# Kernel optimization log

Measured on AMD Instinct MI355X. Metric: run time of the kernel, lower is better.

## Reference

```python
import jax, jax.numpy as jnp
import numpy as np
from jax.nn import relu, softplus, sigmoid

B, T, C, L = 256, 128, 16, 64
ENC, H, OBS_IN, NLAGS = 32, 64, 8, 24
SUBSTEPS = 2


def setup_inputs() -> dict:
    key = jax.random.key(0)
    ks = jax.random.split(key, 32)
    rn = lambda k, shp, s=0.1: jax.random.normal(k, shp, dtype=jnp.float32) * s
    return {
        "timestamps": jnp.linspace(0.0, 1.0, T, dtype=jnp.float32),
        "obs": rn(ks[0], (B, NLAGS, OBS_IN), 1.0),
        "coef_d": rn(ks[1], (B, T - 1, C)),
        "coef_c": rn(ks[2], (B, T - 1, C)),
        "coef_b": rn(ks[3], (B, T - 1, C)),
        "coef_a": rn(ks[4], (B, T - 1, C)),
        "gru_wih": rn(ks[5], (3 * H, OBS_IN)),
        "gru_whh": rn(ks[6], (3 * H, H)),
        "gru_bih": rn(ks[7], (3 * H,)),
        "gru_bhh": rn(ks[8], (3 * H,)),
        "gru_lin_w": rn(ks[9], (ENC, H)),
        "ie_w0": rn(ks[10], (128, ENC + C)),
        "ie_b0": rn(ks[11], (128,)),
        "ie_wh": rn(ks[12], (1, 128, 128)),
        "ie_bh": rn(ks[13], (1, 128)),
        "ie_wout": rn(ks[14], (L, 128)),
        "ie_bout": rn(ks[15], (L,)),
        "vf_w0": rn(ks[16], (128, L)),
        "vf_b0": rn(ks[17], (128,)),
        "vf_wh": rn(ks[18], (1, 128, 128)),
        "vf_bh": rn(ks[19], (1, 128)),
        "vf_wout": rn(ks[20], (L * C, 128)),
        "vf_bout": rn(ks[21], (L * C,)),
        "dec_w0": rn(ks[22], (L // 2, L)),
        "dec_b0": rn(ks[23], (L // 2,)),
        "dec_wh": rn(ks[24], (1, L // 2, L // 2)),
        "dec_bh": rn(ks[25], (1, L // 2)),
        "dec_wout": rn(ks[26], (8, L // 2)),
        "dec_bout": rn(ks[27], (8,)),
    }


def _mlp(x, w0, b0, wh, bh, wout, bout, act, fact):
    h = act(w0 @ x + b0)
    for i in range(wh.shape[0]):  # fixed small depth
        h = act(wh[i] @ h + bh[i])
    return fact(wout @ h + bout)


_ident = lambda v: v


def reference(timestamps, obs, coef_d, coef_c, coef_b, coef_a,
              gru_wih, gru_whh, gru_bih, gru_bhh, gru_lin_w,
              ie_w0, ie_b0, ie_wh, ie_bh, ie_wout, ie_bout,
              vf_w0, vf_b0, vf_wh, vf_bh, vf_wout, vf_bout,
              dec_w0, dec_b0, dec_wh, dec_bh, dec_wout, dec_bout):

    def single(obs_s, d_s, c_s, b_s, a_s):
        # --- GRU observation encoder ---
        def cell(h, x):
            gi = gru_wih @ x + gru_bih
            gh = gru_whh @ h + gru_bhh
            ir, iz, inn = jnp.split(gi, 3)
            hr, hz, hn = jnp.split(gh, 3)
            r = sigmoid(ir + hr)
            z = sigmoid(iz + hz)
            n = jnp.tanh(inn + r * hn)
            return (1.0 - z) * n + z * h, None
        hT, _ = jax.lax.scan(cell, jnp.zeros((H,), jnp.float32), obs_s)
        enc = gru_lin_w @ hT
        # control.evaluate(t0): cubic poly at frac=0 -> constant coeff a[0]
        x0 = a_s[0]
        y0 = _mlp(jnp.concatenate([enc, x0]), ie_w0, ie_b0, ie_wh, ie_bh, ie_wout, ie_bout, relu, _ident)

        def vf(y):
            return _mlp(y, vf_w0, vf_b0, vf_wh, vf_bh, vf_wout, vf_bout, softplus, jnp.tanh).reshape(L, C)

        js = jnp.arange(SUBSTEPS, dtype=jnp.float32)

        def interval(y, xs):
            t0, t1, di, ci, bi = xs
            hstep = (t1 - t0) / SUBSTEPS
            def f(frac, yy):
                dx = bi + 2.0 * ci * frac + 3.0 * di * frac * frac  # dX/dt on this interval
                return vf(yy) @ dx  # (L,)
            def sub(yy, j):  # one fixed Dopri5 step
                f0 = j * hstep
                k1 = f(f0, yy)
                k2 = f(f0 + hstep / 5, yy + hstep * (k1 / 5))
                k3 = f(f0 + 3 * hstep / 10, yy + hstep * (3 / 40 * k1 + 9 / 40 * k2))
                k4 = f(f0 + 4 * hstep / 5, yy + hstep * (44 / 45 * k1 - 56 / 15 * k2 + 32 / 9 * k3))
                k5 = f(f0 + 8 * hstep / 9, yy + hstep * (19372 / 6561 * k1 - 25360 / 2187 * k2 + 64448 / 6561 * k3 - 212 / 729 * k4))
                k6 = f(f0 + hstep, yy + hstep * (9017 / 3168 * k1 - 355 / 33 * k2 + 46732 / 5247 * k3 + 49 / 176 * k4 - 5103 / 18656 * k5))
                yn = yy + hstep * (35 / 384 * k1 + 500 / 1113 * k3 + 125 / 192 * k4 - 2187 / 6784 * k5 + 11 / 84 * k6)
                return yn, None
            y, _ = jax.lax.scan(jax.checkpoint(sub), y, js)
            return y, y

        xs = (timestamps[:-1], timestamps[1:], d_s, c_s, b_s)
        _, ys_rest = jax.lax.scan(interval, y0, xs)
        ys = jnp.concatenate([y0[None], ys_rest], axis=0)  # (T, L)
        dec = lambda yy: _mlp(yy, dec_w0, dec_b0, dec_wh, dec_bh, dec_wout, dec_bout, relu, _ident)
        return jax.vmap(dec)(ys)  # (T, state_size)

    return jax.vmap(single)(obs, coef_d, coef_c, coef_b, coef_a)  # (B, T, state_size)
```

## Files before the change

kernel.cpp:

```cpp
#include <hip/hip_runtime.h>
#include <hip/hip_fp16.h>

#define TPB 512

typedef _Float16 h2v __attribute__((ext_vector_type(2)));

__device__ __forceinline__ float dot2f(unsigned int a, unsigned int b, float c) {
#if __has_builtin(__builtin_amdgcn_fdot2)
    return __builtin_amdgcn_fdot2(__builtin_bit_cast(h2v, a), __builtin_bit_cast(h2v, b), c, false);
#else
    float2 af = __half22float2(__builtin_bit_cast(__half2, a));
    float2 bf = __half22float2(__builtin_bit_cast(__half2, b));
    return fmaf(af.y, bf.y, fmaf(af.x, bf.x, c));
#endif
}

__device__ __forceinline__ unsigned int pack2(float a, float b) {
    unsigned int lo = (unsigned int)__half_as_ushort(__float2half_rn(a));
    unsigned int hi = (unsigned int)__half_as_ushort(__float2half_rn(b));
    return lo | (hi << 16);
}

__device__ __forceinline__ float softplus_f(float x) {
    return fmaxf(x, 0.f) + __logf(1.f + __expf(-fabsf(x)));
}
__device__ __forceinline__ float tanh_f(float x) {
    float e = __expf(2.f * x);
    return 1.f - 2.f / (e + 1.f);
}
__device__ __forceinline__ float sigmoid_f(float x) {
    return 1.f / (1.f + __expf(-x));
}

__global__ __launch_bounds__(TPB, 2) void ncde_kernel(
    const float* __restrict__ timestamps, const float* __restrict__ obs,
    const float* __restrict__ coef_d, const float* __restrict__ coef_c,
    const float* __restrict__ coef_b, const float* __restrict__ coef_a,
    const float* __restrict__ gru_wih, const float* __restrict__ gru_whh,
    const float* __restrict__ gru_bih, const float* __restrict__ gru_bhh,
    const float* __restrict__ gru_lin_w,
    const float* __restrict__ ie_w0, const float* __restrict__ ie_b0,
    const float* __restrict__ ie_wh, const float* __restrict__ ie_bh,
    const float* __restrict__ ie_wout, const float* __restrict__ ie_bout,
    const float* __restrict__ vf_w0, const float* __restrict__ vf_b0,
    const float* __restrict__ vf_wh, const float* __restrict__ vf_bh,
    const float* __restrict__ vf_wout, const float* __restrict__ vf_bout,
    const float* __restrict__ dec_w0, const float* __restrict__ dec_b0,
    const float* __restrict__ dec_wh, const float* __restrict__ dec_bh,
    const float* __restrict__ dec_wout, const float* __restrict__ dec_bout,
    float* __restrict__ out)
{
    const int b = blockIdx.x;
    const int tid = threadIdx.x;

    __shared__ __align__(16) float s_ysall[128][64];
    __shared__ __align__(16) float s_whh[192 * 65];
    __shared__ __align__(16) float s_wih[192 * 9];
    __shared__ __align__(16) float s_obs[24 * 8];
    __shared__ float s_gi[192];
    __shared__ float s_gh[192];
    __shared__ __align__(16) float s_y[64];
    __shared__ __align__(16) float s_ysg[64];
    __shared__ __align__(16) __half s_h1h[128];
    __shared__ __align__(16) __half s_h2h[128];
    __shared__ float s_k[6][64];
    __shared__ float s_bi[16], s_ci[16], s_di[16], s_dx[16];
    __shared__ __align__(16) float s_v48[48];
    __shared__ float s_m1[128], s_m2[128];
    __shared__ float s_A[6][5];
    __shared__ float s_C[6];
    __shared__ float s_Bw[6];

    if (tid == 0) {
        const float A[6][5] = {
            {0.f, 0.f, 0.f, 0.f, 0.f},
            {0.2f, 0.f, 0.f, 0.f, 0.f},
            {3.f / 40.f, 9.f / 40.f, 0.f, 0.f, 0.f},
            {44.f / 45.f, -56.f / 15.f, 32.f / 9.f, 0.f, 0.f},
            {19372.f / 6561.f, -25360.f / 2187.f, 64448.f / 6561.f, -212.f / 729.f, 0.f},
            {9017.f / 3168.f, -355.f / 33.f, 46732.f / 5247.f, 49.f / 176.f, -5103.f / 18656.f}};
        const float C[6] = {0.f, 0.2f, 0.3f, 0.8f, 8.f / 9.f, 1.f};
        const float Bw[6] = {35.f / 384.f, 0.f, 500.f / 1113.f, 125.f / 192.f,
                             -2187.f / 6784.f, 11.f / 84.f};
        for (int i = 0; i < 6; ++i) {
            s_C[i] = C[i];
            s_Bw[i] = Bw[i];
            for (int m = 0; m < 5; ++m) s_A[i][m] = A[i][m];
        }
    }

    for (int idx = tid; idx < 192 * 64; idx += TPB)
        s_whh[(idx >> 6) * 65 + (idx & 63)] = gru_whh[idx];
    for (int idx = tid; idx < 192 * 8; idx += TPB)
        s_wih[(idx >> 3) * 9 + (idx & 7)] = gru_wih[idx];
    for (int idx = tid; idx < 24 * 8; idx += TPB)
        s_obs[idx] = obs[(size_t)b * 192 + idx];
    const float bih_r = (tid < 192) ? gru_bih[tid] : 0.f;
    const float bhh_r = (tid < 192) ? gru_bhh[tid] : 0.f;
    if (tid < 64) s_y[tid] = 0.f;
    __syncthreads();

    for (int step = 0; step < 24; ++step) {
        if (tid < 192) {
            float gi = bih_r;
            const float* wr = &s_wih[tid * 9];
            const float* xr = &s_obs[step * 8];
#pragma unroll
            for (int j = 0; j < 8; ++j) gi = fmaf(wr[j], xr[j], gi);
            float gh = bhh_r;
            const float* hr = &s_whh[tid * 65];
            for (int j = 0; j < 64; ++j) gh = fmaf(hr[j], s_y[j], gh);
            s_gi[tid] = gi;
            s_gh[tid] = gh;
        }
        __syncthreads();
        if (tid < 64) {
            float rg = sigmoid_f(s_gi[tid] + s_gh[tid]);
            float zg = sigmoid_f(s_gi[64 + tid] + s_gh[64 + tid]);
            float ng = tanh_f(s_gi[128 + tid] + rg * s_gh[128 + tid]);
            s_y[tid] = (1.f - zg) * ng + zg * s_y[tid];
        }
        __syncthreads();
    }

    if (tid < 32) {
        float e = 0.f;
        const float* wr = gru_lin_w + tid * 64;
        for (int j = 0; j < 64; ++j) e = fmaf(wr[j], s_y[j], e);
        s_v48[tid] = e;
    } else if (tid < 48) {
        s_v48[tid] = coef_a[(size_t)b * 127 * 16 + (tid - 32)];
    }
    __syncthreads();

    if (tid < 128) {
        float a = ie_b0[tid];
        const float* wr = ie_w0 + tid * 48;
        for (int j = 0; j < 48; ++j) a = fmaf(wr[j], s_v48[j], a);
        s_m1[tid] = fmaxf(a, 0.f);
    }
    __syncthreads();
    if (tid < 128) {
        float a = ie_bh[tid];
        const float* wr = ie_wh + tid * 128;
        for (int j = 0; j < 128; ++j) a = fmaf(wr[j], s_m1[j], a);
        s_m2[tid] = fmaxf(a, 0.f);
    }
    __syncthreads();
    if (tid < 64) {
        float a = ie_bout[tid];
        const float* wr = ie_wout + tid * 128;
        for (int j = 0; j < 128; ++j) a = fmaf(wr[j], s_m2[j], a);
        s_y[tid] = a;
        s_ysall[0][tid] = a;
    }
    __syncthreads();

    const int qrow = tid >> 2, qc = tid & 3;
    float w0_r[16];
    {
        const float* base = vf_w0 + qrow * 64 + qc * 16;
#pragma unroll
        for (int j = 0; j < 16; ++j) w0_r[j] = base[j];
    }
    unsigned int wh_r[16];
    {
        const float* base = vf_wh + qrow * 128 + qc * 32;
#pragma unroll
        for (int j = 0; j < 16; ++j) wh_r[j] = pack2(base[2 * j], base[2 * j + 1]);
    }
    unsigned int wq0[64], wq1[64];
    {
        const float* r0 = vf_wout + (size_t)(2 * tid) * 128;
#pragma unroll
        for (int j = 0; j < 64; ++j) wq0[j] = pack2(r0[2 * j], r0[2 * j + 1]);
        const float* r1 = r0 + 128;
#pragma unroll
        for (int j = 0; j < 64; ++j) wq1[j] = pack2(r1[2 * j], r1[2 * j + 1]);
    }
    const float b0_r = vf_b0[qrow];
    const float bh_r = vf_bh[qrow];
    const float bo0 = vf_bout[2 * tid], bo1 = vf_bout[2 * tid + 1];
    const int l_idx = tid >> 3;
    const int c0 = 2 * (tid & 7);

    const size_t cofs = (size_t)b * 127 * 16;

#pragma unroll 1
    for (int t = 0; t < 127; ++t) {
        if (tid < 16) s_bi[tid] = coef_b[cofs + t * 16 + tid];
        else if (tid < 32) s_ci[tid - 16] = coef_c[cofs + t * 16 + (tid - 16)];
        else if (tid < 48) s_di[tid - 32] = coef_d[cofs + t * 16 + (tid - 32)];
        const float t0 = timestamps[t], t1 = timestamps[t + 1];
        const float hstep = (t1 - t0) * 0.5f;
        __syncthreads();

#pragma unroll 1
        for (int sub = 0; sub < 2; ++sub) {
            const float f0 = (float)sub * hstep;
#pragma unroll 1
            for (int s = 0; s < 6; ++s) {
                if (tid < 64) {
                    float yv = s_y[tid];
                    for (int m = 0; m < s; ++m)
                        yv = fmaf(hstep * s_A[s][m], s_k[m][tid], yv);
                    s_ysg[tid] = yv;
                } else if (tid < 80) {
                    int c = tid - 64;
                    float frac = fmaf(s_C[s], hstep, f0);
                    s_dx[c] = fmaf(3.f * s_di[c], frac * frac,
                                   fmaf(2.f * s_ci[c], frac, s_bi[c]));
                }
                __syncthreads();

                {
                    float a = 0.f;
                    const float* yb = &s_ysg[qc * 16];
#pragma unroll
                    for (int k4 = 0; k4 < 4; ++k4) {
                        float4 yv = *reinterpret_cast<const float4*>(yb + 4 * k4);
                        a = fmaf(w0_r[4 * k4 + 0], yv.x, a);
                        a = fmaf(w0_r[4 * k4 + 1], yv.y, a);
                        a = fmaf(w0_r[4 * k4 + 2], yv.z, a);
                        a = fmaf(w0_r[4 * k4 + 3], yv.w, a);
                    }
                    a += __shfl_xor(a, 1);
                    a += __shfl_xor(a, 2);
                    if (qc == 0) s_h1h[qrow] = __float2half_rn(softplus_f(a + b0_r));
                }
                __syncthreads();

                {
                    float a = 0.f;
                    const __half* hb = &s_h1h[qc * 32];
#pragma unroll
                    for (int k4 = 0; k4 < 4; ++k4) {
                        uint4 hv = *reinterpret_cast<const uint4*>(hb + 8 * k4);
                        a = dot2f(wh_r[4 * k4 + 0], hv.x, a);
                        a = dot2f(wh_r[4 * k4 + 1], hv.y, a);
                        a = dot2f(wh_r[4 * k4 + 2], hv.z, a);
                        a = dot2f(wh_r[4 * k4 + 3], hv.w, a);
                    }
                    a += __shfl_xor(a, 1);
                    a += __shfl_xor(a, 2);
                    if (qc == 0) s_h2h[qrow] = __float2half_rn(softplus_f(a + bh_r));
                }
                __syncthreads();

                {
                    float a0 = 0.f, a1 = 0.f;
#pragma unroll
                    for (int k4 = 0; k4 < 16; ++k4) {
                        uint4 hv = *reinterpret_cast<const uint4*>(&s_h2h[8 * k4]);
                        a0 = dot2f(wq0[4 * k4 + 0], hv.x, a0);
                        a1 = dot2f(wq1[4 * k4 + 0], hv.x, a1);
                        a0 = dot2f(wq0[4 * k4 + 1], hv.y, a0);
                        a1 = dot2f(wq1[4 * k4 + 1], hv.y, a1);
                        a0 = dot2f(wq0[4 * k4 + 2], hv.z, a0);
                        a1 = dot2f(wq1[4 * k4 + 2], hv.z, a1);
                        a0 = dot2f(wq0[4 * k4 + 3], hv.w, a0);
                        a1 = dot2f(wq1[4 * k4 + 3], hv.w, a1);
                    }
                    float v0 = tanh_f(a0 + bo0);
                    float v1 = tanh_f(a1 + bo1);
                    float p = v0 * s_dx[c0] + v1 * s_dx[c0 + 1];
                    p += __shfl_xor(p, 1);
                    p += __shfl_xor(p, 2);
                    p += __shfl_xor(p, 4);
                    if ((tid & 7) == 0) s_k[s][l_idx] = p;
                }
                __syncthreads();
            }

            if (tid < 64) {
                float yv = s_y[tid];
#pragma unroll
                for (int m = 0; m < 6; ++m)
                    yv = fmaf(hstep * s_Bw[m], s_k[m][tid], yv);
                s_y[tid] = yv;
                if (sub == 1) s_ysall[t + 1][tid] = yv;
            }
            __syncthreads();
        }
    }

    const int wid = tid >> 6, lane = tid & 63;
    for (int t = wid; t < 128; t += 8) {
        const float* yy = s_ysall[t];
        float h1d = 0.f;
        if (lane < 32) {
            float a = dec_b0[lane];
            const float* wr = dec_w0 + lane * 64;
            for (int j = 0; j < 64; ++j) a = fmaf(wr[j], yy[j], a);
            h1d = fmaxf(a, 0.f);
        }
        float a2 = (lane < 32) ? dec_bh[lane] : 0.f;
#pragma unroll 8
        for (int j = 0; j < 32; ++j) {
            float hj = __shfl(h1d, j);
            if (lane < 32) a2 = fmaf(dec_wh[lane * 32 + j], hj, a2);
        }
        float h2d = fmaxf(a2, 0.f);
        float o = (lane < 8) ? dec_bout[lane] : 0.f;
#pragma unroll 8
        for (int j = 0; j < 32; ++j) {
            float hj = __shfl(h2d, j);
            if (lane < 8) o = fmaf(dec_wout[lane * 32 + j], hj, o);
        }
        if (lane < 8) out[(size_t)b * 1024 + t * 8 + lane] = o;
    }
}

extern "C" void kernel_launch(void* const* d_in, const int* in_sizes, int n_in,
                              void* d_out, int out_size, void* d_ws, size_t ws_size,
                              hipStream_t stream) {
    const float* p[29];
    for (int i = 0; i < 29; ++i) p[i] = (const float*)d_in[i];
    ncde_kernel<<<256, TPB, 0, stream>>>(
        p[0], p[1], p[2], p[3], p[4], p[5], p[6], p[7], p[8], p[9], p[10],
        p[11], p[12], p[13], p[14], p[15], p[16], p[17], p[18], p[19], p[20],
        p[21], p[22], p[23], p[24], p[25], p[26], p[27], p[28],
        (float*)d_out);
}
```

Measured before the change: 2.705 ms.

## Double block to 1024 threads, one vf_wout row per thread, drop a barrier

The block grows from 512 to 1024 threads, and each thread now holds a single fp16 vf_wout row instead of two. This roughly halves per-thread register weight storage and serial dot-product length. The first two MLP layers use 8-way splits per row. The control derivative dx is computed inline per thread instead of through a separate shared-memory stage, and the stage-0 y copy is written at the end of the previous step, which removes one barrier per RK stage. The GRU loop uses four accumulators. The cost is more warps contending at every __syncthreads, plus higher per-block resource pressure under the new launch bounds.

```diff
diff --git a/kernel.cpp b/kernel.cpp
--- a/kernel.cpp
+++ b/kernel.cpp
@@ -1,7 +1,7 @@
 #include <hip/hip_runtime.h>
 #include <hip/hip_fp16.h>
 
-#define TPB 512
+#define TPB 1024
 
 typedef _Float16 h2v __attribute__((ext_vector_type(2)));
 
@@ -32,7 +32,7 @@
     return 1.f / (1.f + __expf(-x));
 }
 
-__global__ __launch_bounds__(TPB, 2) void ncde_kernel(
+__global__ __launch_bounds__(TPB, 4) void ncde_kernel(
     const float* __restrict__ timestamps, const float* __restrict__ obs,
     const float* __restrict__ coef_d, const float* __restrict__ coef_c,
     const float* __restrict__ coef_b, const float* __restrict__ coef_a,
@@ -64,7 +64,7 @@
     __shared__ __align__(16) __half s_h1h[128];
     __shared__ __align__(16) __half s_h2h[128];
     __shared__ float s_k[6][64];
-    __shared__ float s_bi[16], s_ci[16], s_di[16], s_dx[16];
+    __shared__ float s_bi[16], s_ci[16], s_di[16];
     __shared__ __align__(16) float s_v48[48];
     __shared__ float s_m1[128], s_m2[128];
     __shared__ float s_A[6][5];
@@ -93,8 +93,7 @@
         s_whh[(idx >> 6) * 65 + (idx & 63)] = gru_whh[idx];
     for (int idx = tid; idx < 192 * 8; idx += TPB)
         s_wih[(idx >> 3) * 9 + (idx & 7)] = gru_wih[idx];
-    for (int idx = tid; idx < 24 * 8; idx += TPB)
-        s_obs[idx] = obs[(size_t)b * 192 + idx];
+    if (tid < 24 * 8) s_obs[tid] = obs[(size_t)b * 192 + tid];
     const float bih_r = (tid < 192) ? gru_bih[tid] : 0.f;
     const float bhh_r = (tid < 192) ? gru_bhh[tid] : 0.f;
     if (tid < 64) s_y[tid] = 0.f;
@@ -107,11 +106,17 @@
             const float* xr = &s_obs[step * 8];
 #pragma unroll
             for (int j = 0; j < 8; ++j) gi = fmaf(wr[j], xr[j], gi);
-            float gh = bhh_r;
+            float g0 = bhh_r, g1 = 0.f, g2 = 0.f, g3 = 0.f;
             const float* hr = &s_whh[tid * 65];
-            for (int j = 0; j < 64; ++j) gh = fmaf(hr[j], s_y[j], gh);
+#pragma unroll 4
+            for (int j = 0; j < 64; j += 4) {
+                g0 = fmaf(hr[j + 0], s_y[j + 0], g0);
+                g1 = fmaf(hr[j + 1], s_y[j + 1], g1);
+                g2 = fmaf(hr[j + 2], s_y[j + 2], g2);
+                g3 = fmaf(hr[j + 3], s_y[j + 3], g3);
+            }
             s_gi[tid] = gi;
-            s_gh[tid] = gh;
+            s_gh[tid] = (g0 + g1) + (g2 + g3);
         }
         __syncthreads();
         if (tid < 64) {
@@ -152,37 +157,35 @@
         const float* wr = ie_wout + tid * 128;
         for (int j = 0; j < 128; ++j) a = fmaf(wr[j], s_m2[j], a);
         s_y[tid] = a;
+        s_ysg[tid] = a;
         s_ysall[0][tid] = a;
     }
     __syncthreads();
 
-    const int qrow = tid >> 2, qc = tid & 3;
-    float w0_r[16];
+    const int row8 = tid >> 3, seg8 = tid & 7;
+    float w0_r[8];
     {
-        const float* base = vf_w0 + qrow * 64 + qc * 16;
-#pragma unroll
-        for (int j = 0; j < 16; ++j) w0_r[j] = base[j];
-    }
-    unsigned int wh_r[16];
+        const float* base = vf_w0 + row8 * 64 + seg8 * 8;
+#pragma unroll
+        for (int j = 0; j < 8; ++j) w0_r[j] = base[j];
+    }
+    unsigned int wh_r[8];
     {
-        const float* base = vf_wh + qrow * 128 + qc * 32;
-#pragma unroll
-        for (int j = 0; j < 16; ++j) wh_r[j] = pack2(base[2 * j], base[2 * j + 1]);
-    }
-    unsigned int wq0[64], wq1[64];
+        const float* base = vf_wh + row8 * 128 + seg8 * 16;
+#pragma unroll
+        for (int j = 0; j < 8; ++j) wh_r[j] = pack2(base[2 * j], base[2 * j + 1]);
+    }
+    unsigned int wq[64];
     {
-        const float* r0 = vf_wout + (size_t)(2 * tid) * 128;
-#pragma unroll
-        for (int j = 0; j < 64; ++j) wq0[j] = pack2(r0[2 * j], r0[2 * j + 1]);
-        const float* r1 = r0 + 128;
-#pragma unroll
-        for (int j = 0; j < 64; ++j) wq1[j] = pack2(r1[2 * j], r1[2 * j + 1]);
-    }
-    const float b0_r = vf_b0[qrow];
-    const float bh_r = vf_bh[qrow];
-    const float bo0 = vf_bout[2 * tid], bo1 = vf_bout[2 * tid + 1];
-    const int l_idx = tid >> 3;
-    const int c0 = 2 * (tid & 7);
+        const float* r0 = vf_wout + (size_t)tid * 128;
+#pragma unroll
+        for (int j = 0; j < 64; ++j) wq[j] = pack2(r0[2 * j], r0[2 * j + 1]);
+    }
+    const float b0_r = vf_b0[row8];
+    const float bh_r = vf_bh[row8];
+    const float bo = vf_bout[tid];
+    const int l_idx = tid >> 4;
+    const int c_idx = tid & 15;
 
     const size_t cofs = (size_t)b * 127 * 16;
 
@@ -200,74 +203,75 @@
             const float f0 = (float)sub * hstep;
 #pragma unroll 1
             for (int s = 0; s < 6; ++s) {
-                if (tid < 64) {
-                    float yv = s_y[tid];
-                    for (int m = 0; m < s; ++m)
-                        yv = fmaf(hstep * s_A[s][m], s_k[m][tid], yv);
-                    s_ysg[tid] = yv;
-                } else if (tid < 80) {
-                    int c = tid - 64;
-                    float frac = fmaf(s_C[s], hstep, f0);
-                    s_dx[c] = fmaf(3.f * s_di[c], frac * frac,
-                                   fmaf(2.f * s_ci[c], frac, s_bi[c]));
+                if (s > 0) {
+                    if (tid < 64) {
+                        float yv = s_y[tid];
+                        for (int m = 0; m < s; ++m)
+                            yv = fmaf(hstep * s_A[s][m], s_k[m][tid], yv);
+                        s_ysg[tid] = yv;
+                    }
+                    __syncthreads();
+                }
+
+                {
+                    const float* yb = &s_ysg[seg8 * 8];
+                    float4 y0 = *reinterpret_cast<const float4*>(yb);
+                    float4 y1 = *reinterpret_cast<const float4*>(yb + 4);
+                    float a0 = w0_r[0] * y0.x, a1 = w0_r[1] * y0.y;
+                    a0 = fmaf(w0_r[2], y0.z, a0);
+                    a1 = fmaf(w0_r[3], y0.w, a1);
+                    a0 = fmaf(w0_r[4], y1.x, a0);
+                    a1 = fmaf(w0_r[5], y1.y, a1);
+                    a0 = fmaf(w0_r[6], y1.z, a0);
+                    a1 = fmaf(w0_r[7], y1.w, a1);
+                    float a = a0 + a1;
+                    a += __shfl_xor(a, 1);
+                    a += __shfl_xor(a, 2);
+                    a += __shfl_xor(a, 4);
+                    if (seg8 == 0) s_h1h[row8] = __float2half_rn(softplus_f(a + b0_r));
                 }
                 __syncthreads();
 
                 {
-                    float a = 0.f;
-                    const float* yb = &s_ysg[qc * 16];
-#pragma unroll
-                    for (int k4 = 0; k4 < 4; ++k4) {
-                        float4 yv = *reinterpret_cast<const float4*>(yb + 4 * k4);
-                        a = fmaf(w0_r[4 * k4 + 0], yv.x, a);
-                        a = fmaf(w0_r[4 * k4 + 1], yv.y, a);
-                        a = fmaf(w0_r[4 * k4 + 2], yv.z, a);
-                        a = fmaf(w0_r[4 * k4 + 3], yv.w, a);
-                    }
+                    const __half* hb = &s_h1h[seg8 * 16];
+                    uint4 h0 = *reinterpret_cast<const uint4*>(hb);
+                    uint4 h1v = *reinterpret_cast<const uint4*>(hb + 8);
+                    float a0 = dot2f(wh_r[0], h0.x, 0.f);
+                    float a1 = dot2f(wh_r[1], h0.y, 0.f);
+                    a0 = dot2f(wh_r[2], h0.z, a0);
+                    a1 = dot2f(wh_r[3], h0.w, a1);
+                    a0 = dot2f(wh_r[4], h1v.x, a0);
+                    a1 = dot2f(wh_r[5], h1v.y, a1);
+                    a0 = dot2f(wh_r[6], h1v.z, a0);
+                    a1 = dot2f(wh_r[7], h1v.w, a1);
+                    float a = a0 + a1;
                     a += __shfl_xor(a, 1);
                     a += __shfl_xor(a, 2);
-                    if (qc == 0) s_h1h[qrow] = __float2half_rn(softplus_f(a + b0_r));
+                    a += __shfl_xor(a, 4);
+                    if (seg8 == 0) s_h2h[row8] = __float2half_rn(softplus_f(a + bh_r));
                 }
                 __syncthreads();
 
                 {
-                    float a = 0.f;
-                    const __half* hb = &s_h1h[qc * 32];
-#pragma unroll
-                    for (int k4 = 0; k4 < 4; ++k4) {
-                        uint4 hv = *reinterpret_cast<const uint4*>(hb + 8 * k4);
-                        a = dot2f(wh_r[4 * k4 + 0], hv.x, a);
-                        a = dot2f(wh_r[4 * k4 + 1], hv.y, a);
-                        a = dot2f(wh_r[4 * k4 + 2], hv.z, a);
-                        a = dot2f(wh_r[4 * k4 + 3], hv.w, a);
-                    }
-                    a += __shfl_xor(a, 1);
-                    a += __shfl_xor(a, 2);
-                    if (qc == 0) s_h2h[qrow] = __float2half_rn(softplus_f(a + bh_r));
-                }
-                __syncthreads();
-
-                {
-                    float a0 = 0.f, a1 = 0.f;
+                    float a0 = 0.f, a1 = 0.f, a2 = 0.f, a3 = 0.f;
 #pragma unroll
                     for (int k4 = 0; k4 < 16; ++k4) {
                         uint4 hv = *reinterpret_cast<const uint4*>(&s_h2h[8 * k4]);
-                        a0 = dot2f(wq0[4 * k4 + 0], hv.x, a0);
-                        a1 = dot2f(wq1[4 * k4 + 0], hv.x, a1);
-                        a0 = dot2f(wq0[4 * k4 + 1], hv.y, a0);
-                        a1 = dot2f(wq1[4 * k4 + 1], hv.y, a1);
-                        a0 = dot2f(wq0[4 * k4 + 2], hv.z, a0);
-                        a1 = dot2f(wq1[4 * k4 + 2], hv.z, a1);
-                        a0 = dot2f(wq0[4 * k4 + 3], hv.w, a0);
-                        a1 = dot2f(wq1[4 * k4 + 3], hv.w, a1);
+                        a0 = dot2f(wq[4 * k4 + 0], hv.x, a0);
+                        a1 = dot2f(wq[4 * k4 + 1], hv.y, a1);
+                        a2 = dot2f(wq[4 * k4 + 2], hv.z, a2);
+                        a3 = dot2f(wq[4 * k4 + 3], hv.w, a3);
                     }
-                    float v0 = tanh_f(a0 + bo0);
-                    float v1 = tanh_f(a1 + bo1);
-                    float p = v0 * s_dx[c0] + v1 * s_dx[c0 + 1];
+                    float v = tanh_f((a0 + a1) + (a2 + a3) + bo);
+                    float frac = fmaf(s_C[s], hstep, f0);
+                    float dx = fmaf(3.f * s_di[c_idx], frac * frac,
+                                    fmaf(2.f * s_ci[c_idx], frac, s_bi[c_idx]));
+                    float p = v * dx;
                     p += __shfl_xor(p, 1);
                     p += __shfl_xor(p, 2);
                     p += __shfl_xor(p, 4);
-                    if ((tid & 7) == 0) s_k[s][l_idx] = p;
+                    p += __shfl_xor(p, 8);
+                    if (c_idx == 0) s_k[s][l_idx] = p;
                 }
                 __syncthreads();
             }
@@ -278,6 +282,7 @@
                 for (int m = 0; m < 6; ++m)
                     yv = fmaf(hstep * s_Bw[m], s_k[m][tid], yv);
                 s_y[tid] = yv;
+                s_ysg[tid] = yv;
                 if (sub == 1) s_ysall[t + 1][tid] = yv;
             }
             __syncthreads();
@@ -285,7 +290,7 @@
     }
 
     const int wid = tid >> 6, lane = tid & 63;
-    for (int t = wid; t < 128; t += 8) {
+    for (int t = wid; t < 128; t += 16) {
         const float* yy = s_ysall[t];
         float h1d = 0.f;
         if (lane < 32) {
```

Measured after the change: 3.438 ms. 27.1% more time.

## Batch 16 samples per block and run vector-field MLP on MFMA

Applied to the files above, without the earlier changes.

Each block now handles 16 batch samples instead of one, so grid size drops to 16 blocks. The three vector-field matvecs become 16x16x32 f16 MFMA matmuls, with weights kept in registers as fragments and activations stored in swizzled shared memory. The GRU encoder, initial MLP and per-step decoder are also batched, and decoding now runs inside the time loop. This amortises weights and barriers over 16 samples, but it leaves most CUs idle and puts a longer dependent chain in each block.

```diff
diff --git a/kernel.cpp b/kernel.cpp
--- a/kernel.cpp
+++ b/kernel.cpp
@@ -2,24 +2,10 @@
 #include <hip/hip_fp16.h>
 
 #define TPB 512
-
-typedef _Float16 h2v __attribute__((ext_vector_type(2)));
-
-__device__ __forceinline__ float dot2f(unsigned int a, unsigned int b, float c) {
-#if __has_builtin(__builtin_amdgcn_fdot2)
-    return __builtin_amdgcn_fdot2(__builtin_bit_cast(h2v, a), __builtin_bit_cast(h2v, b), c, false);
-#else
-    float2 af = __half22float2(__builtin_bit_cast(__half2, a));
-    float2 bf = __half22float2(__builtin_bit_cast(__half2, b));
-    return fmaf(af.y, bf.y, fmaf(af.x, bf.x, c));
-#endif
-}
-
-__device__ __forceinline__ unsigned int pack2(float a, float b) {
-    unsigned int lo = (unsigned int)__half_as_ushort(__float2half_rn(a));
-    unsigned int hi = (unsigned int)__half_as_ushort(__float2half_rn(b));
-    return lo | (hi << 16);
-}
+#define NB 16
+
+typedef _Float16 f16x8 __attribute__((ext_vector_type(8)));
+typedef float f32x4 __attribute__((ext_vector_type(4)));
 
 __device__ __forceinline__ float softplus_f(float x) {
     return fmaxf(x, 0.f) + __logf(1.f + __expf(-fabsf(x)));
@@ -32,7 +18,11 @@
     return 1.f / (1.f + __expf(-x));
 }
 
-__global__ __launch_bounds__(TPB, 2) void ncde_kernel(
+__device__ __forceinline__ f32x4 mfma16(f16x8 a, f16x8 b, f32x4 c) {
+    return __builtin_amdgcn_mfma_f32_16x16x32_f16(a, b, c, 0, 0, 0);
+}
+
+__global__ __launch_bounds__(TPB, 1) void ncde_kernel(
     const float* __restrict__ timestamps, const float* __restrict__ obs,
     const float* __restrict__ coef_d, const float* __restrict__ coef_c,
     const float* __restrict__ coef_b, const float* __restrict__ coef_a,
@@ -50,264 +40,344 @@
     const float* __restrict__ dec_wout, const float* __restrict__ dec_bout,
     float* __restrict__ out)
 {
-    const int b = blockIdx.x;
     const int tid = threadIdx.x;
-
-    __shared__ __align__(16) float s_ysall[128][64];
-    __shared__ __align__(16) float s_whh[192 * 65];
-    __shared__ __align__(16) float s_wih[192 * 9];
-    __shared__ __align__(16) float s_obs[24 * 8];
-    __shared__ float s_gi[192];
-    __shared__ float s_gh[192];
-    __shared__ __align__(16) float s_y[64];
-    __shared__ __align__(16) float s_ysg[64];
-    __shared__ __align__(16) __half s_h1h[128];
-    __shared__ __align__(16) __half s_h2h[128];
-    __shared__ float s_k[6][64];
-    __shared__ float s_bi[16], s_ci[16], s_di[16], s_dx[16];
-    __shared__ __align__(16) float s_v48[48];
-    __shared__ float s_m1[128], s_m2[128];
-    __shared__ float s_A[6][5];
-    __shared__ float s_C[6];
-    __shared__ float s_Bw[6];
-
-    if (tid == 0) {
-        const float A[6][5] = {
-            {0.f, 0.f, 0.f, 0.f, 0.f},
-            {0.2f, 0.f, 0.f, 0.f, 0.f},
-            {3.f / 40.f, 9.f / 40.f, 0.f, 0.f, 0.f},
-            {44.f / 45.f, -56.f / 15.f, 32.f / 9.f, 0.f, 0.f},
-            {19372.f / 6561.f, -25360.f / 2187.f, 64448.f / 6561.f, -212.f / 729.f, 0.f},
-            {9017.f / 3168.f, -355.f / 33.f, 46732.f / 5247.f, 49.f / 176.f, -5103.f / 18656.f}};
-        const float C[6] = {0.f, 0.2f, 0.3f, 0.8f, 8.f / 9.f, 1.f};
-        const float Bw[6] = {35.f / 384.f, 0.f, 500.f / 1113.f, 125.f / 192.f,
-                             -2187.f / 6784.f, 11.f / 84.f};
-        for (int i = 0; i < 6; ++i) {
-            s_C[i] = C[i];
-            s_Bw[i] = Bw[i];
-            for (int m = 0; m < 5; ++m) s_A[i][m] = A[i][m];
-        }
-    }
+    const int b0 = blockIdx.x * NB;
+    const int lane = tid & 63, wv = tid >> 6;
+    const int m16 = lane & 15, g4 = lane >> 4;
+
+    __shared__ __align__(16) char s_pool[85504];
+    float* const s_whh = (float*)(s_pool);
+    float* const s_wih = (float*)(s_pool + 49920);
+    float* const s_obs = (float*)(s_pool + 56832);
+    float* const s_gsum = (float*)(s_pool + 69120);
+    float* const s_ghn = (float*)(s_pool + 81408);
+    float* const s_v48 = (float*)(s_pool);
+    float* const s_m1 = (float*)(s_pool + 3072);
+    float* const s_m2 = (float*)(s_pool + 11264);
+    float* const s_k = (float*)(s_pool);
+    char* const s_ysb = s_pool + 24576;
+    char* const s_h1 = s_pool + 26624;
+    char* const s_h2 = s_pool + 30720;
+    char* const s_dxT = s_pool + 34816;
+    float* const s_cb = (float*)(s_pool + 35840);
+    float* const s_cc = (float*)(s_pool + 36864);
+    float* const s_cd = (float*)(s_pool + 37888);
+    float* const s_bout = (float*)(s_pool + 38912);
+
+    __shared__ __align__(16) float s_h[NB * 64];
+    __shared__ __align__(16) float s_y[NB * 64];
+    __shared__ float s_bih[192], s_bhh[192];
+    __shared__ __align__(16) float s_dw0[32 * 65];
+    __shared__ __align__(16) float s_dwh[32 * 33];
+    __shared__ __align__(16) float s_dwo[8 * 33];
+    __shared__ float s_db0[32], s_dbh[32], s_dbo[8];
 
     for (int idx = tid; idx < 192 * 64; idx += TPB)
         s_whh[(idx >> 6) * 65 + (idx & 63)] = gru_whh[idx];
     for (int idx = tid; idx < 192 * 8; idx += TPB)
         s_wih[(idx >> 3) * 9 + (idx & 7)] = gru_wih[idx];
-    for (int idx = tid; idx < 24 * 8; idx += TPB)
-        s_obs[idx] = obs[(size_t)b * 192 + idx];
-    const float bih_r = (tid < 192) ? gru_bih[tid] : 0.f;
-    const float bhh_r = (tid < 192) ? gru_bhh[tid] : 0.f;
-    if (tid < 64) s_y[tid] = 0.f;
+    for (int idx = tid; idx < NB * 192; idx += TPB)
+        s_obs[idx] = obs[(size_t)b0 * 192 + idx];
+    if (tid < 192) { s_bih[tid] = gru_bih[tid]; s_bhh[tid] = gru_bhh[tid]; }
+    for (int idx = tid; idx < NB * 64; idx += TPB) s_h[idx] = 0.f;
+    for (int idx = tid; idx < 2048; idx += TPB)
+        s_dw0[(idx >> 6) * 65 + (idx & 63)] = dec_w0[idx];
+    for (int idx = tid; idx < 1024; idx += TPB)
+        s_dwh[(idx >> 5) * 33 + (idx & 31)] = dec_wh[idx];
+    if (tid < 256) s_dwo[(tid >> 5) * 33 + (tid & 31)] = dec_wout[tid];
+    if (tid < 32) { s_db0[tid] = dec_b0[tid]; s_dbh[tid] = dec_bh[tid]; }
+    if (tid < 8) s_dbo[tid] = dec_bout[tid];
     __syncthreads();
 
     for (int step = 0; step < 24; ++step) {
-        if (tid < 192) {
-            float gi = bih_r;
-            const float* wr = &s_wih[tid * 9];
-            const float* xr = &s_obs[step * 8];
+#pragma unroll
+        for (int i = 0; i < 6; ++i) {
+            const int item = tid + i * TPB;
+            const int bb = item / 192, g = item - bb * 192;
+            float gi = s_bih[g];
+            const float* wr = &s_wih[g * 9];
+            const float* xr = &s_obs[bb * 192 + step * 8];
 #pragma unroll
             for (int j = 0; j < 8; ++j) gi = fmaf(wr[j], xr[j], gi);
-            float gh = bhh_r;
-            const float* hr = &s_whh[tid * 65];
-            for (int j = 0; j < 64; ++j) gh = fmaf(hr[j], s_y[j], gh);
-            s_gi[tid] = gi;
-            s_gh[tid] = gh;
-        }
-        __syncthreads();
-        if (tid < 64) {
-            float rg = sigmoid_f(s_gi[tid] + s_gh[tid]);
-            float zg = sigmoid_f(s_gi[64 + tid] + s_gh[64 + tid]);
-            float ng = tanh_f(s_gi[128 + tid] + rg * s_gh[128 + tid]);
-            s_y[tid] = (1.f - zg) * ng + zg * s_y[tid];
-        }
-        __syncthreads();
-    }
-
-    if (tid < 32) {
+            float a0 = s_bhh[g], a1 = 0.f, a2 = 0.f, a3 = 0.f;
+            const float* hr = &s_whh[g * 65];
+            const float* hb = &s_h[bb * 64];
+#pragma unroll 4
+            for (int j = 0; j < 64; j += 4) {
+                a0 = fmaf(hr[j + 0], hb[j + 0], a0);
+                a1 = fmaf(hr[j + 1], hb[j + 1], a1);
+                a2 = fmaf(hr[j + 2], hb[j + 2], a2);
+                a3 = fmaf(hr[j + 3], hb[j + 3], a3);
+            }
+            float gh = (a0 + a1) + (a2 + a3);
+            if (g < 128) s_gsum[bb * 192 + g] = gi + gh;
+            else { s_gsum[bb * 192 + g] = gi; s_ghn[bb * 64 + g - 128] = gh; }
+        }
+        __syncthreads();
+#pragma unroll
+        for (int i = 0; i < 2; ++i) {
+            const int item = tid + i * TPB;
+            const int bb = item >> 6, j = item & 63;
+            float rg = sigmoid_f(s_gsum[bb * 192 + j]);
+            float zg = sigmoid_f(s_gsum[bb * 192 + 64 + j]);
+            float ng = tanh_f(s_gsum[bb * 192 + 128 + j] + rg * s_ghn[bb * 64 + j]);
+            s_h[bb * 64 + j] = (1.f - zg) * ng + zg * s_h[bb * 64 + j];
+        }
+        __syncthreads();
+    }
+
+    {
+        const int bb = tid >> 5, r = tid & 31;
         float e = 0.f;
-        const float* wr = gru_lin_w + tid * 64;
-        for (int j = 0; j < 64; ++j) e = fmaf(wr[j], s_y[j], e);
-        s_v48[tid] = e;
-    } else if (tid < 48) {
-        s_v48[tid] = coef_a[(size_t)b * 127 * 16 + (tid - 32)];
-    }
-    __syncthreads();
-
-    if (tid < 128) {
-        float a = ie_b0[tid];
-        const float* wr = ie_w0 + tid * 48;
-        for (int j = 0; j < 48; ++j) a = fmaf(wr[j], s_v48[j], a);
-        s_m1[tid] = fmaxf(a, 0.f);
-    }
-    __syncthreads();
-    if (tid < 128) {
-        float a = ie_bh[tid];
-        const float* wr = ie_wh + tid * 128;
-        for (int j = 0; j < 128; ++j) a = fmaf(wr[j], s_m1[j], a);
-        s_m2[tid] = fmaxf(a, 0.f);
-    }
-    __syncthreads();
-    if (tid < 64) {
-        float a = ie_bout[tid];
-        const float* wr = ie_wout + tid * 128;
-        for (int j = 0; j < 128; ++j) a = fmaf(wr[j], s_m2[j], a);
-        s_y[tid] = a;
-        s_ysall[0][tid] = a;
-    }
-    __syncthreads();
-
-    const int qrow = tid >> 2, qc = tid & 3;
-    float w0_r[16];
+        const float* wr = gru_lin_w + r * 64;
+        const float* hb = s_h + bb * 64;
+#pragma unroll 8
+        for (int j = 0; j < 64; ++j) e = fmaf(wr[j], hb[j], e);
+        s_v48[bb * 48 + r] = e;
+    }
+    if (tid < 256) {
+        const int bb = tid >> 4, c = tid & 15;
+        s_v48[bb * 48 + 32 + c] = coef_a[(size_t)(b0 + bb) * 2032 + c];
+    }
+    __syncthreads();
+#pragma unroll
+    for (int i = 0; i < 4; ++i) {
+        const int item = tid + i * TPB;
+        const int bb = item >> 7, r = item & 127;
+        float a = ie_b0[r];
+        const float* wr = ie_w0 + r * 48;
+        const float* vb = s_v48 + bb * 48;
+#pragma unroll 8
+        for (int j = 0; j < 48; ++j) a = fmaf(wr[j], vb[j], a);
+        s_m1[bb * 128 + r] = fmaxf(a, 0.f);
+    }
+    __syncthreads();
+#pragma unroll
+    for (int i = 0; i < 4; ++i) {
+        const int item = tid + i * TPB;
+        const int bb = item >> 7, r = item & 127;
+        float a = ie_bh[r];
+        const float* wr = ie_wh + r * 128;
+        const float* vb = s_m1 + bb * 128;
+#pragma unroll 8
+        for (int j = 0; j < 128; ++j) a = fmaf(wr[j], vb[j], a);
+        s_m2[bb * 128 + r] = fmaxf(a, 0.f);
+    }
+    __syncthreads();
+#pragma unroll
+    for (int i = 0; i < 2; ++i) {
+        const int item = tid + i * TPB;
+        const int bb = item >> 6, r = item & 63;
+        float a = ie_bout[r];
+        const float* wr = ie_wout + r * 128;
+        const float* vb = s_m2 + bb * 128;
+#pragma unroll 8
+        for (int j = 0; j < 128; ++j) a = fmaf(wr[j], vb[j], a);
+        s_y[bb * 64 + r] = a;
+    }
+    __syncthreads();
+
+    f16x8 aw0[2], awh[4], awq[8][4];
     {
-        const float* base = vf_w0 + qrow * 64 + qc * 16;
-#pragma unroll
-        for (int j = 0; j < 16; ++j) w0_r[j] = base[j];
-    }
-    unsigned int wh_r[16];
-    {
-        const float* base = vf_wh + qrow * 128 + qc * 32;
-#pragma unroll
-        for (int j = 0; j < 16; ++j) wh_r[j] = pack2(base[2 * j], base[2 * j + 1]);
-    }
-    unsigned int wq0[64], wq1[64];
-    {
-        const float* r0 = vf_wout + (size_t)(2 * tid) * 128;
-#pragma unroll
-        for (int j = 0; j < 64; ++j) wq0[j] = pack2(r0[2 * j], r0[2 * j + 1]);
-        const float* r1 = r0 + 128;
-#pragma unroll
-        for (int j = 0; j < 64; ++j) wq1[j] = pack2(r1[2 * j], r1[2 * j + 1]);
-    }
-    const float b0_r = vf_b0[qrow];
-    const float bh_r = vf_bh[qrow];
-    const float bo0 = vf_bout[2 * tid], bo1 = vf_bout[2 * tid + 1];
-    const int l_idx = tid >> 3;
-    const int c0 = 2 * (tid & 7);
-
-    const size_t cofs = (size_t)b * 127 * 16;
+        const int row = wv * 16 + m16;
+#pragma unroll
+        for (int f = 0; f < 2; ++f) {
+            f16x8 a;
+#pragma unroll
+            for (int j = 0; j < 8; ++j)
+                a[j] = (_Float16)vf_w0[row * 64 + f * 32 + g4 * 8 + j];
+            aw0[f] = a;
+        }
+#pragma unroll
+        for (int f = 0; f < 4; ++f) {
+            f16x8 a;
+#pragma unroll
+            for (int j = 0; j < 8; ++j)
+                a[j] = (_Float16)vf_wh[row * 128 + f * 32 + g4 * 8 + j];
+            awh[f] = a;
+        }
+#pragma unroll
+        for (int i = 0; i < 8; ++i) {
+            const int rq = (wv * 8 + i) * 16 + m16;
+#pragma unroll
+            for (int f = 0; f < 4; ++f) {
+                f16x8 a;
+#pragma unroll
+                for (int j = 0; j < 8; ++j)
+                    a[j] = (_Float16)vf_wout[(size_t)rq * 128 + f * 32 + g4 * 8 + j];
+                awq[i][f] = a;
+            }
+        }
+    }
+    const float4 bw0 = *(const float4*)(vf_b0 + wv * 16 + g4 * 4);
+    const float4 bwh = *(const float4*)(vf_bh + wv * 16 + g4 * 4);
+    for (int idx = tid; idx < 1024; idx += TPB) s_bout[idx] = vf_bout[idx];
+
+    auto decode_t = [&](int t) {
+        const int job = wv * 2 + (lane >> 5);
+        const int ln = lane & 31;
+        const float* yy = s_y + job * 64;
+        float a = s_db0[ln];
+#pragma unroll 8
+        for (int j = 0; j < 64; ++j) a = fmaf(s_dw0[ln * 65 + j], yy[j], a);
+        float h1d = fmaxf(a, 0.f);
+        float a2 = s_dbh[ln];
+#pragma unroll 8
+        for (int j = 0; j < 32; ++j) a2 = fmaf(s_dwh[ln * 33 + j], __shfl(h1d, j, 32), a2);
+        float h2d = fmaxf(a2, 0.f);
+        float o = (ln < 8) ? s_dbo[ln] : 0.f;
+#pragma unroll 8
+        for (int j = 0; j < 32; ++j) {
+            float hj = __shfl(h2d, j, 32);
+            if (ln < 8) o = fmaf(s_dwo[ln * 33 + j], hj, o);
+        }
+        if (ln < 8) out[(size_t)(b0 + job) * 1024 + t * 8 + ln] = o;
+    };
+
+    auto stage_bcd = [&](int S) {
+        const int swz = (m16 & 7) << 4;
+        {
+            f16x8 bf0 = *(const f16x8*)(s_ysb + ((m16 * 128 + g4 * 16) ^ swz));
+            f16x8 bf1 = *(const f16x8*)(s_ysb + ((m16 * 128 + 64 + g4 * 16) ^ swz));
+            f32x4 acc = {0.f, 0.f, 0.f, 0.f};
+            acc = mfma16(aw0[0], bf0, acc);
+            acc = mfma16(aw0[1], bf1, acc);
+            __half h0 = __float2half_rn(softplus_f(acc[0] + bw0.x));
+            __half h1v = __float2half_rn(softplus_f(acc[1] + bw0.y));
+            __half h2v = __float2half_rn(softplus_f(acc[2] + bw0.z));
+            __half h3v = __float2half_rn(softplus_f(acc[3] + bw0.w));
+            uint2 pk;
+            pk.x = (unsigned)__half_as_ushort(h0) | ((unsigned)__half_as_ushort(h1v) << 16);
+            pk.y = (unsigned)__half_as_ushort(h2v) | ((unsigned)__half_as_ushort(h3v) << 16);
+            *(uint2*)(s_h1 + ((m16 * 256 + (wv * 16 + g4 * 4) * 2) ^ swz)) = pk;
+        }
+        __syncthreads();
+        {
+            f16x8 bf[4];
+#pragma unroll
+            for (int f = 0; f < 4; ++f)
+                bf[f] = *(const f16x8*)(s_h1 + ((m16 * 256 + f * 64 + g4 * 16) ^ swz));
+            f32x4 acc = {0.f, 0.f, 0.f, 0.f};
+#pragma unroll
+            for (int f = 0; f < 4; ++f) acc = mfma16(awh[f], bf[f], acc);
+            __half h0 = __float2half_rn(softplus_f(acc[0] + bwh.x));
+            __half h1v = __float2half_rn(softplus_f(acc[1] + bwh.y));
+            __half h2v = __float2half_rn(softplus_f(acc[2] + bwh.z));
+            __half h3v = __float2half_rn(softplus_f(acc[3] + bwh.w));
+            uint2 pk;
+            pk.x = (unsigned)__half_as_ushort(h0) | ((unsigned)__half_as_ushort(h1v) << 16);
+            pk.y = (unsigned)__half_as_ushort(h2v) | ((unsigned)__half_as_ushort(h3v) << 16);
+            *(uint2*)(s_h2 + ((m16 * 256 + (wv * 16 + g4 * 4) * 2) ^ swz)) = pk;
+        }
+        __syncthreads();
+        {
+            f16x8 bf[4];
+#pragma unroll
+            for (int f = 0; f < 4; ++f)
+                bf[f] = *(const f16x8*)(s_h2 + ((m16 * 256 + f * 64 + g4 * 16) ^ swz));
+            const float4 dx4 = *(const float4*)(s_dxT + ((m16 * 64 + g4 * 16) ^ ((m16 & 3) << 4)));
+#pragma unroll
+            for (int i = 0; i < 8; ++i) {
+                f32x4 acc = {0.f, 0.f, 0.f, 0.f};
+#pragma unroll
+                for (int f = 0; f < 4; ++f) acc = mfma16(awq[i][f], bf[f], acc);
+                const float4 bo = *(const float4*)(s_bout + (wv * 8 + i) * 16 + g4 * 4);
+                float p = tanh_f(acc[0] + bo.x) * dx4.x;
+                p = fmaf(tanh_f(acc[1] + bo.y), dx4.y, p);
+                p = fmaf(tanh_f(acc[2] + bo.z), dx4.z, p);
+                p = fmaf(tanh_f(acc[3] + bo.w), dx4.w, p);
+                p += __shfl_xor(p, 16);
+                p += __shfl_xor(p, 32);
+                if (g4 == 0) s_k[(S * 64 + wv * 8 + i) * 16 + m16] = p;
+            }
+        }
+        __syncthreads();
+    };
+
+#define KS(m) s_k[((m) * 64 + kk) * 16 + bb]
+#define PHASE_A(CC, ...)                                                       \
+    {                                                                          \
+        _Pragma("unroll")                                                      \
+        for (int it = 0; it < 2; ++it) {                                       \
+            const int item = tid + it * TPB;                                   \
+            const int bb = item >> 6, kk = item & 63;                          \
+            float yv = s_y[bb * 64 + kk];                                      \
+            __VA_ARGS__                                                        \
+            *(unsigned short*)(s_ysb + ((bb * 128 + kk * 2) ^ ((bb & 7) << 4))) = \
+                __half_as_ushort(__float2half_rn(yv));                         \
+        }                                                                      \
+        if (tid < 256) {                                                       \
+            const int bb = tid >> 4;                                           \
+            const float frac = fmaf((CC), hstep, f0);                          \
+            const float dv = fmaf(3.f * s_cd[tid], frac * frac,                \
+                                  fmaf(2.f * s_cc[tid], frac, s_cb[tid]));     \
+            *(float*)(s_dxT + ((bb * 64 + (tid & 15) * 4) ^ ((bb & 3) << 4))) = dv; \
+        }                                                                      \
+        __syncthreads();                                                       \
+    }
+
+    if (tid < 256) {
+        const size_t o = (size_t)(b0 + (tid >> 4)) * 2032 + (tid & 15);
+        s_cb[tid] = coef_b[o];
+        s_cd[tid] = coef_d[o];
+    } else {
+        const int i2 = tid - 256;
+        s_cc[i2] = coef_c[(size_t)(b0 + (i2 >> 4)) * 2032 + (i2 & 15)];
+    }
+    decode_t(0);
+    __syncthreads();
 
 #pragma unroll 1
     for (int t = 0; t < 127; ++t) {
-        if (tid < 16) s_bi[tid] = coef_b[cofs + t * 16 + tid];
-        else if (tid < 32) s_ci[tid - 16] = coef_c[cofs + t * 16 + (tid - 16)];
-        else if (tid < 48) s_di[tid - 32] = coef_d[cofs + t * 16 + (tid - 32)];
-        const float t0 = timestamps[t], t1 = timestamps[t + 1];
-        const float hstep = (t1 - t0) * 0.5f;
-        __syncthreads();
-
+        const float hstep = (timestamps[t + 1] - timestamps[t]) * 0.5f;
 #pragma unroll 1
         for (int sub = 0; sub < 2; ++sub) {
             const float f0 = (float)sub * hstep;
-#pragma unroll 1
-            for (int s = 0; s < 6; ++s) {
-                if (tid < 64) {
-                    float yv = s_y[tid];
-                    for (int m = 0; m < s; ++m)
-                        yv = fmaf(hstep * s_A[s][m], s_k[m][tid], yv);
-                    s_ysg[tid] = yv;
-                } else if (tid < 80) {
-                    int c = tid - 64;
-                    float frac = fmaf(s_C[s], hstep, f0);
-                    s_dx[c] = fmaf(3.f * s_di[c], frac * frac,
-                                   fmaf(2.f * s_ci[c], frac, s_bi[c]));
+
+            PHASE_A(0.f, ;)
+            stage_bcd(0);
+            PHASE_A(0.2f, yv = fmaf(hstep * 0.2f, KS(0), yv);)
+            stage_bcd(1);
+            PHASE_A(0.3f, yv = fmaf(hstep, fmaf(3.f / 40.f, KS(0), (9.f / 40.f) * KS(1)), yv);)
+            stage_bcd(2);
+            PHASE_A(0.8f, yv = fmaf(hstep, fmaf(44.f / 45.f, KS(0),
+                          fmaf(-56.f / 15.f, KS(1), (32.f / 9.f) * KS(2))), yv);)
+            stage_bcd(3);
+            PHASE_A(8.f / 9.f, yv = fmaf(hstep, fmaf(19372.f / 6561.f, KS(0),
+                          fmaf(-25360.f / 2187.f, KS(1),
+                          fmaf(64448.f / 6561.f, KS(2), (-212.f / 729.f) * KS(3)))), yv);)
+            stage_bcd(4);
+            PHASE_A(1.f, yv = fmaf(hstep, fmaf(9017.f / 3168.f, KS(0),
+                          fmaf(-355.f / 33.f, KS(1),
+                          fmaf(46732.f / 5247.f, KS(2),
+                          fmaf(49.f / 176.f, KS(3), (-5103.f / 18656.f) * KS(4))))), yv);)
+            stage_bcd(5);
+
+#pragma unroll
+            for (int it = 0; it < 2; ++it) {
+                const int item = tid + it * TPB;
+                const int bb = item >> 6, kk = item & 63;
+                float yv = s_y[bb * 64 + kk];
+                yv = fmaf(hstep * (35.f / 384.f), KS(0), yv);
+                yv = fmaf(hstep * (500.f / 1113.f), KS(2), yv);
+                yv = fmaf(hstep * (125.f / 192.f), KS(3), yv);
+                yv = fmaf(hstep * (-2187.f / 6784.f), KS(4), yv);
+                yv = fmaf(hstep * (11.f / 84.f), KS(5), yv);
+                s_y[bb * 64 + kk] = yv;
+            }
+            if (sub == 1 && t < 126) {
+                if (tid < 256) {
+                    const size_t o = (size_t)(b0 + (tid >> 4)) * 2032 + (t + 1) * 16 + (tid & 15);
+                    s_cb[tid] = coef_b[o];
+                    s_cd[tid] = coef_d[o];
+                } else {
+                    const int i2 = tid - 256;
+                    s_cc[i2] = coef_c[(size_t)(b0 + (i2 >> 4)) * 2032 + (t + 1) * 16 + (i2 & 15)];
                 }
-                __syncthreads();
-
-                {
-                    float a = 0.f;
-                    const float* yb = &s_ysg[qc * 16];
-#pragma unroll
-                    for (int k4 = 0; k4 < 4; ++k4) {
-                        float4 yv = *reinterpret_cast<const float4*>(yb + 4 * k4);
-                        a = fmaf(w0_r[4 * k4 + 0], yv.x, a);
-                        a = fmaf(w0_r[4 * k4 + 1], yv.y, a);
-                        a = fmaf(w0_r[4 * k4 + 2], yv.z, a);
-                        a = fmaf(w0_r[4 * k4 + 3], yv.w, a);
-                    }
-                    a += __shfl_xor(a, 1);
-                    a += __shfl_xor(a, 2);
-                    if (qc == 0) s_h1h[qrow] = __float2half_rn(softplus_f(a + b0_r));
-                }
-                __syncthreads();
-
-                {
-                    float a = 0.f;
-                    const __half* hb = &s_h1h[qc * 32];
-#pragma unroll
-                    for (int k4 = 0; k4 < 4; ++k4) {
-                        uint4 hv = *reinterpret_cast<const uint4*>(hb + 8 * k4);
-                        a = dot2f(wh_r[4 * k4 + 0], hv.x, a);
-                        a = dot2f(wh_r[4 * k4 + 1], hv.y, a);
-                        a = dot2f(wh_r[4 * k4 + 2], hv.z, a);
-                        a = dot2f(wh_r[4 * k4 + 3], hv.w, a);
-                    }
-                    a += __shfl_xor(a, 1);
-                    a += __shfl_xor(a, 2);
-                    if (qc == 0) s_h2h[qrow] = __float2half_rn(softplus_f(a + bh_r));
-                }
-                __syncthreads();
-
-                {
-                    float a0 = 0.f, a1 = 0.f;
-#pragma unroll
-                    for (int k4 = 0; k4 < 16; ++k4) {
-                        uint4 hv = *reinterpret_cast<const uint4*>(&s_h2h[8 * k4]);
-                        a0 = dot2f(wq0[4 * k4 + 0], hv.x, a0);
-                        a1 = dot2f(wq1[4 * k4 + 0], hv.x, a1);
-                        a0 = dot2f(wq0[4 * k4 + 1], hv.y, a0);
-                        a1 = dot2f(wq1[4 * k4 + 1], hv.y, a1);
-                        a0 = dot2f(wq0[4 * k4 + 2], hv.z, a0);
-                        a1 = dot2f(wq1[4 * k4 + 2], hv.z, a1);
-                        a0 = dot2f(wq0[4 * k4 + 3], hv.w, a0);
-                        a1 = dot2f(wq1[4 * k4 + 3], hv.w, a1);
-                    }
-                    float v0 = tanh_f(a0 + bo0);
-                    float v1 = tanh_f(a1 + bo1);
-                    float p = v0 * s_dx[c0] + v1 * s_dx[c0 + 1];
-                    p += __shfl_xor(p, 1);
-                    p += __shfl_xor(p, 2);
-                    p += __shfl_xor(p, 4);
-                    if ((tid & 7) == 0) s_k[s][l_idx] = p;
-                }
-                __syncthreads();
-            }
-
-            if (tid < 64) {
-                float yv = s_y[tid];
-#pragma unroll
-                for (int m = 0; m < 6; ++m)
-                    yv = fmaf(hstep * s_Bw[m], s_k[m][tid], yv);
-                s_y[tid] = yv;
-                if (sub == 1) s_ysall[t + 1][tid] = yv;
             }
             __syncthreads();
         }
-    }
-
-    const int wid = tid >> 6, lane = tid & 63;
-    for (int t = wid; t < 128; t += 8) {
-        const float* yy = s_ysall[t];
-        float h1d = 0.f;
-        if (lane < 32) {
-            float a = dec_b0[lane];
-            const float* wr = dec_w0 + lane * 64;
-            for (int j = 0; j < 64; ++j) a = fmaf(wr[j], yy[j], a);
-            h1d = fmaxf(a, 0.f);
-        }
-        float a2 = (lane < 32) ? dec_bh[lane] : 0.f;
-#pragma unroll 8
-        for (int j = 0; j < 32; ++j) {
-            float hj = __shfl(h1d, j);
-            if (lane < 32) a2 = fmaf(dec_wh[lane * 32 + j], hj, a2);
-        }
-        float h2d = fmaxf(a2, 0.f);
-        float o = (lane < 8) ? dec_bout[lane] : 0.f;
-#pragma unroll 8
-        for (int j = 0; j < 32; ++j) {
-            float hj = __shfl(h2d, j);
-            if (lane < 8) o = fmaf(dec_wout[lane * 32 + j], hj, o);
-        }
-        if (lane < 8) out[(size_t)b * 1024 + t * 8 + lane] = o;
+        decode_t(t + 1);
     }
 }
 
@@ -316,7 +386,7 @@
                               hipStream_t stream) {
     const float* p[29];
     for (int i = 0; i < 29; ++i) p[i] = (const float*)d_in[i];
-    ncde_kernel<<<256, TPB, 0, stream>>>(
+    ncde_kernel<<<256 / NB, TPB, 0, stream>>>(
         p[0], p[1], p[2], p[3], p[4], p[5], p[6], p[7], p[8], p[9], p[10],
         p[11], p[12], p[13], p[14], p[15], p[16], p[17], p[18], p[19], p[20],
         p[21], p[22], p[23], p[24], p[25], p[26], p[27], p[28],
```

Result: slower. 7.562 ms (+179.6%).
